# Optimization experiments

Measured on AMD Instinct MI355X. Metric: run time of the kernel, lower is better.

The kernel has to match this reference:

```python
import jax, jax.numpy as jnp
import numpy as np

BIG = jnp.float32(9e15)


def _normalize(sim, mask):
    # min/max are taken over positions where mask == 0 (faithful to the torch code)
    mn = jnp.min(jnp.where(mask == 0.0, sim, BIG), axis=-1, keepdims=True)
    mx = jnp.max(jnp.where(mask == 0.0, sim, -BIG), axis=-1, keepdims=True)
    return (sim - mn) / (mx - mn)


def setup_inputs() -> dict:
    key = jax.random.key(0)
    k1, k2 = jax.random.split(key)
    B, M = 4096, 8192
    return {
        "similarity_matrix": jax.random.normal(k1, (B, B), dtype=jnp.float32),
        "memory_bank_matrix": jax.random.normal(k2, (B, M), dtype=jnp.float32),
        "num_neighbors": 32,
        "temperature": jnp.ones((), dtype=jnp.float32),
    }


def reference(similarity_matrix, memory_bank_matrix, num_neighbors, temperature):
    sim = similarity_matrix
    B = sim.shape[0]
    eye = jnp.eye(B, dtype=sim.dtype)

    # --- neighbor masks via top-k over off-diagonal similarities ---
    sim_noself = jnp.where(eye == 0.0, sim, -BIG)
    _, topk_idx = jax.lax.top_k(sim_noself, num_neighbors)       # [B, k]
    rows = jnp.broadcast_to(jnp.arange(B)[:, None], topk_idx.shape)
    neighbor_mask = jnp.zeros((B, B), dtype=sim.dtype).at[rows, topk_idx].set(1.0)
    extended_mask = eye.at[rows, topk_idx].set(1.0)

    # --- centrality from memory bank ---
    centrality = jnp.mean(memory_bank_matrix, axis=-1)           # [B]
    cent_exp = jnp.broadcast_to(centrality[None, :], (B, B))

    norm_sim = _normalize(sim, extended_mask)
    norm_cent = _normalize(cent_exp, extended_mask)

    adjusted = jnp.where(neighbor_mask == 1.0, norm_sim - norm_cent, -BIG)

    # --- positive weights ---
    pw = jax.nn.softmax(adjusted * temperature, axis=-1)
    pw = jnp.where(neighbor_mask == 1.0, pw, 0.0)
    pw = jnp.where(eye == 1.0, 1.0, pw)  # fill_diagonal_(1.0)

    # --- masked log-softmax loss ---
    masked_sim = jnp.where(extended_mask == 1.0, sim, -BIG)
    logp = jax.nn.log_softmax(masked_sim, axis=-1) * pw
    per_row = -jnp.sum(logp, axis=-1) / jnp.sum(pw, axis=-1)
    return jnp.mean(per_row)
```

## Files before the change

kernel.cpp:

```cpp
#include <hip/hip_runtime.h>
#include <cmath>


#define CAP 256
#define MAXIT 40

__device__ inline float wave_max_f(float x) {
#pragma unroll
    for (int off = 32; off > 0; off >>= 1) x = fmaxf(x, __shfl_xor(x, off, 64));
    return x;
}
__device__ inline float wave_min_f(float x) {
#pragma unroll
    for (int off = 32; off > 0; off >>= 1) x = fminf(x, __shfl_xor(x, off, 64));
    return x;
}
__device__ inline float wave_sum_f(float x) {
#pragma unroll
    for (int off = 32; off > 0; off >>= 1) x += __shfl_xor(x, off, 64);
    return x;
}
__device__ inline unsigned int wave_min_u32(unsigned int x) {
#pragma unroll
    for (int off = 32; off > 0; off >>= 1) {
        unsigned int o = (unsigned int)__shfl_xor((int)x, off, 64);
        x = (o < x) ? o : x;
    }
    return x;
}

__device__ inline unsigned int f_to_key(float f) {
    unsigned int u = __float_as_uint(f);
    return u ^ ((u & 0x80000000u) ? 0xFFFFFFFFu : 0x80000000u);
}
__device__ inline float key_to_f(unsigned int key) {
    unsigned int u = key ^ ((key & 0x80000000u) ? 0x80000000u : 0xFFFFFFFFu);
    return __uint_as_float(u);
}

__device__ inline unsigned int lane_prefix(unsigned long long mask) {
    return __builtin_amdgcn_mbcnt_hi((unsigned int)(mask >> 32),
           __builtin_amdgcn_mbcnt_lo((unsigned int)mask, 0u));
}

__global__ __launch_bounds__(256)
void cent_kernel(const float* __restrict__ mem, float* __restrict__ cent, int M) {
    __shared__ float s[4];
    const int row = blockIdx.x;
    const float4* p = (const float4*)(mem + (size_t)row * M);
    const int n4 = M >> 2;
    float acc = 0.0f;
    int i = threadIdx.x;
    for (; i + 1792 < n4; i += 2048) {
        float4 q0 = p[i], q1 = p[i + 256], q2 = p[i + 512], q3 = p[i + 768];
        float4 q4 = p[i + 1024], q5 = p[i + 1280], q6 = p[i + 1536], q7 = p[i + 1792];
        acc += ((q0.x + q0.y) + (q0.z + q0.w)) + ((q1.x + q1.y) + (q1.z + q1.w))
             + ((q2.x + q2.y) + (q2.z + q2.w)) + ((q3.x + q3.y) + (q3.z + q3.w))
             + ((q4.x + q4.y) + (q4.z + q4.w)) + ((q5.x + q5.y) + (q5.z + q5.w))
             + ((q6.x + q6.y) + (q6.z + q6.w)) + ((q7.x + q7.y) + (q7.z + q7.w));
    }
    for (; i < n4; i += 256) {
        float4 q = p[i];
        acc += (q.x + q.y) + (q.z + q.w);
    }
    acc = wave_sum_f(acc);
    const int lane = threadIdx.x & 63, wid = threadIdx.x >> 6;
    if (lane == 0) s[wid] = acc;
    __syncthreads();
    if (threadIdx.x == 0) cent[row] = (s[0] + s[1] + s[2] + s[3]) / (float)M;
}

__global__ __launch_bounds__(256)
void row_loss_kernel(const float* __restrict__ sim,
                     const float* __restrict__ cent,
                     const int* __restrict__ knn,
                     const float* __restrict__ temp_p,
                     float* __restrict__ per_row, int B) {
    __shared__ __align__(16) unsigned long long cand[CAP];
    __shared__ unsigned long long s_sel[64];
    __shared__ unsigned long long s_p33;
    __shared__ unsigned int s_kmin[4];
    __shared__ float s_cmin[4], s_cmax[4];
    __shared__ float s_cmin2[4], s_cmax2[4];
    __shared__ unsigned int s_wcnt[4];
    __shared__ float s_diag;

    const int row = blockIdx.x, tid = threadIdx.x;
    const int lane = tid & 63, wid = tid >> 6;
    const int   k    = knn[0];
    const float temp = temp_p[0];

    const float4* rp = (const float4*)(sim + (size_t)row * B);
    const float4* cp = (const float4*)cent;
    float4 q0 = rp[tid], q1 = rp[256 + tid], q2 = rp[512 + tid], q3 = rp[768 + tid];
    float4 v0 = cp[tid], v1 = cp[256 + tid], v2 = cp[512 + tid], v3 = cp[768 + tid];

    unsigned int keys[16];
    float cv[16];
    unsigned int kmin = 0xFFFFFFFFu;
    {
        float t[16] = {q0.x, q0.y, q0.z, q0.w, q1.x, q1.y, q1.z, q1.w,
                       q2.x, q2.y, q2.z, q2.w, q3.x, q3.y, q3.z, q3.w};
        float c[16] = {v0.x, v0.y, v0.z, v0.w, v1.x, v1.y, v1.z, v1.w,
                       v2.x, v2.y, v2.z, v2.w, v3.x, v3.y, v3.z, v3.w};
#pragma unroll
        for (int c4i = 0; c4i < 4; ++c4i) {
#pragma unroll
            for (int m = 0; m < 4; ++m) {
                const int e = c4i * 4 + m;
                const int j = c4i * 1024 + tid * 4 + m;
                unsigned int key = f_to_key(t[e]);
                if (j == row) { s_diag = t[e]; key = 0u; }
                else if (key < kmin) kmin = key;
                keys[e] = key;
                cv[e] = c[e];
            }
        }
    }
    { unsigned int w = wave_min_u32(kmin); if (lane == 0) s_kmin[wid] = w; }

    unsigned int keyT = f_to_key(2.0f), loK = 0u, hiK = 0xFFFFFFFFu, cnt = 0;
    const unsigned int need = (unsigned int)k + 1u;
    for (int it = 0; it < MAXIT; ++it) {
        float cmin = INFINITY, cmax = -INFINITY;
        unsigned int wvCnt = 0;
#pragma unroll
        for (int e = 0; e < 16; ++e) {
            const unsigned int key = keys[e];
            const bool p = (key > keyT);
            const unsigned long long mask = __ballot(p);
            wvCnt += (unsigned int)__popcll(mask);
            if (!p && key != 0u) {
                cmin = fminf(cmin, cv[e]);
                cmax = fmaxf(cmax, cv[e]);
            }
        }
        { float a = wave_min_f(cmin), b = wave_max_f(cmax);
          if (lane == 0) { s_cmin[wid] = a; s_cmax[wid] = b; s_wcnt[wid] = wvCnt; } }
        __syncthreads();
        cnt = s_wcnt[0] + s_wcnt[1] + s_wcnt[2] + s_wcnt[3];
        if (cnt >= need && cnt <= CAP) break;
        if (it == MAXIT - 1) break;
        if (cnt < need) { hiK = keyT; keyT = loK + ((keyT - loK) >> 1); }
        else            { loK = keyT; keyT = keyT + ((hiK - keyT) >> 1); }
        __syncthreads();
    }

    {
        unsigned int base = 0;
#pragma unroll
        for (int w = 0; w < 4; ++w) if (w < wid) base += s_wcnt[w];
        unsigned int run = 0;
#pragma unroll
        for (int e = 0; e < 16; ++e) {
            const unsigned int key = keys[e];
            const bool p = (key > keyT);
            const unsigned long long mask = __ballot(p);
            if (p) {
                const unsigned int pos = base + run + lane_prefix(mask);
                if (pos < CAP)
                    cand[pos] = ((unsigned long long)key << 32) |
                                (unsigned long long)(0xFFFFFFFFu -
                                    (unsigned int)((e >> 2) * 1024 + tid * 4 + (e & 3)));
            }
            run += (unsigned int)__popcll(mask);
        }
        if (tid == 0) s_p33 = ((unsigned long long)1u) << 32;
        __syncthreads();
    }

    {
        const unsigned int n = min(cnt, (unsigned int)CAP);
        const unsigned int uk = (unsigned int)k;
        float cmin2 = INFINITY, cmax2 = -INFINITY;
        if ((unsigned int)(wid << 6) < n) {
            unsigned long long own = 0ull;
            if ((unsigned int)tid < n) own = cand[tid];
            unsigned int r = 0;
            const ulonglong2* c2 = (const ulonglong2*)cand;
            const unsigned int nq = n >> 2;
            for (unsigned int o = 0; o < nq; ++o) {
                ulonglong2 a0 = c2[2 * o], a1 = c2[2 * o + 1];
                r += (a0.x > own) ? 1u : 0u; r += (a0.y > own) ? 1u : 0u;
                r += (a1.x > own) ? 1u : 0u; r += (a1.y > own) ? 1u : 0u;
            }
            for (unsigned int i = nq << 2; i < n; ++i)
                r += (cand[i] > own) ? 1u : 0u;

            if ((unsigned int)tid < n) {
                if (r < uk) s_sel[r] = own;
                else if (r == uk) s_p33 = own;
                if (r >= uk) {
                    const int jj = (int)(0xFFFFFFFFu - (unsigned int)own);
                    const float cvv = cent[jj];
                    cmin2 = fminf(cmin2, cvv);
                    cmax2 = fmaxf(cmax2, cvv);
                }
            }
        }
        cmin2 = wave_min_f(cmin2);
        cmax2 = wave_max_f(cmax2);
        if (lane == 0) { s_cmin2[wid] = cmin2; s_cmax2[wid] = cmax2; }
        __syncthreads();
    }
    if (wid != 0) return;

    {
        const float sdiag = s_diag;
        const bool  act = (lane < k);
        const unsigned long long sel = act ? s_sel[lane] : 0ull;
        const float sj = act ? key_to_f((unsigned int)(sel >> 32)) : -INFINITY;
        const int   j  = act ? (int)(0xFFFFFFFFu - (unsigned int)sel) : 0;
        const float cj = cent[j];

        const float mn_c = fminf(
            fminf(fminf(s_cmin2[0], s_cmin2[1]), fminf(s_cmin2[2], s_cmin2[3])),
            fminf(fminf(s_cmin[0], s_cmin[1]), fminf(s_cmin[2], s_cmin[3])));
        const float mx_c = fmaxf(
            fmaxf(fmaxf(s_cmax2[0], s_cmax2[1]), fmaxf(s_cmax2[2], s_cmax2[3])),
            fmaxf(fmaxf(s_cmax[0], s_cmax[1]), fmaxf(s_cmax[2], s_cmax[3])));
        const unsigned int kminb =
            min(min(s_kmin[0], s_kmin[1]), min(s_kmin[2], s_kmin[3]));
        const float mn_s = key_to_f(kminb);
        const float mx_s = key_to_f((unsigned int)(s_p33 >> 32));

        float a = -INFINITY;
        if (act) {
            const float ns = (sj - mn_s) / (mx_s - mn_s);
            const float nc = (cj - mn_c) / (mx_c - mn_c);
            a = (ns - nc) * temp;
        }
        const float am   = wave_max_f(a);
        const float e    = act ? expf(a - am) : 0.0f;
        const float esum = wave_sum_f(e);
        const float pw   = e / esum;

        const float m2  = fmaxf(wave_max_f(sj), sdiag);
        const float ex  = act ? expf(sj - m2) : 0.0f;
        const float lse = m2 + logf(wave_sum_f(ex) + expf(sdiag - m2));

        const float num = wave_sum_f(act ? pw * (sj - lse) : 0.0f) + (sdiag - lse);
        const float den = 1.0f + wave_sum_f(pw);
        if (lane == 0) per_row[row] = -num / den;
    }
}

__global__ __launch_bounds__(256)
void reduce_kernel(const float* __restrict__ per_row, float* __restrict__ out, int B) {
    __shared__ float s[4];
    float acc = 0.0f;
    const float4* p = (const float4*)per_row;
    const int n4 = B >> 2;
    for (int i = threadIdx.x; i < n4; i += 256) {
        float4 q = p[i];
        acc += (q.x + q.y) + (q.z + q.w);
    }
    acc = wave_sum_f(acc);
    const int lane = threadIdx.x & 63, wid = threadIdx.x >> 6;
    if (lane == 0) s[wid] = acc;
    __syncthreads();
    if (threadIdx.x == 0) out[0] = (s[0] + s[1] + s[2] + s[3]) / (float)B;
}

extern "C" void kernel_launch(void* const* d_in, const int* in_sizes, int n_in,
                              void* d_out, int out_size, void* d_ws, size_t ws_size,
                              hipStream_t stream) {
    const float* sim  = (const float*)d_in[0];
    const float* mem  = (const float*)d_in[1];
    const int*   knn  = (const int*)d_in[2];
    const float* temp = (const float*)d_in[3];
    float* out     = (float*)d_out;
    float* cent    = (float*)d_ws;
    float* per_row = (float*)d_ws + 4096;

    const int B = (int)(std::sqrt((double)in_sizes[0]) + 0.5);
    const int M = in_sizes[1] / B;

    cent_kernel<<<B, 256, 0, stream>>>(mem, cent, M);
    row_loss_kernel<<<B, 256, 0, stream>>>(sim, cent, knn, temp, per_row, B);
    reduce_kernel<<<1, 256, 0, stream>>>(per_row, out, B);
}
```

Baseline: 51.73 us.

## Fuse first threshold pass with per-wave candidate compaction to skip extra sync

The first threshold count pass now writes candidates directly into per-wave 64-entry segments of the candidate buffer, with the initial threshold raised to 2.2. When the count lands in range and every wave fits its segment, the separate compaction pass and its barrier are skipped, and ranking walks the segments. The binary search runs only as a fallback. The row max for the log-sum-exp is also taken from the top selected key instead of a wave reduction. The cost is more branching and a data-dependent fast path tuned to the normal-distributed test data.

Result: faster. 50.63 us (-2.1%).

```diff
diff --git a/kernel.cpp b/kernel.cpp
--- a/kernel.cpp
+++ b/kernel.cpp
@@ -118,10 +118,11 @@
         }
     }
     { unsigned int w = wave_min_u32(kmin); if (lane == 0) s_kmin[wid] = w; }
-
-    unsigned int keyT = f_to_key(2.0f), loK = 0u, hiK = 0xFFFFFFFFu, cnt = 0;
+    if (tid == 0) s_p33 = ((unsigned long long)1u) << 32;
+
+    unsigned int keyT = f_to_key(2.2f), cnt = 0;
     const unsigned int need = (unsigned int)k + 1u;
-    for (int it = 0; it < MAXIT; ++it) {
+    {
         float cmin = INFINITY, cmax = -INFINITY;
         unsigned int wvCnt = 0;
 #pragma unroll
@@ -129,24 +130,55 @@
             const unsigned int key = keys[e];
             const bool p = (key > keyT);
             const unsigned long long mask = __ballot(p);
-            wvCnt += (unsigned int)__popcll(mask);
-            if (!p && key != 0u) {
+            if (p) {
+                const unsigned int pos = wvCnt + lane_prefix(mask);
+                if (pos < 64u)
+                    cand[(wid << 6) + pos] = ((unsigned long long)key << 32) |
+                        (unsigned long long)(0xFFFFFFFFu -
+                            (unsigned int)((e >> 2) * 1024 + tid * 4 + (e & 3)));
+            } else if (key != 0u) {
                 cmin = fminf(cmin, cv[e]);
                 cmax = fmaxf(cmax, cv[e]);
             }
-        }
-        { float a = wave_min_f(cmin), b = wave_max_f(cmax);
-          if (lane == 0) { s_cmin[wid] = a; s_cmax[wid] = b; s_wcnt[wid] = wvCnt; } }
-        __syncthreads();
-        cnt = s_wcnt[0] + s_wcnt[1] + s_wcnt[2] + s_wcnt[3];
-        if (cnt >= need && cnt <= CAP) break;
-        if (it == MAXIT - 1) break;
-        if (cnt < need) { hiK = keyT; keyT = loK + ((keyT - loK) >> 1); }
-        else            { loK = keyT; keyT = keyT + ((hiK - keyT) >> 1); }
-        __syncthreads();
-    }
-
-    {
+            wvCnt += (unsigned int)__popcll(mask);
+        }
+        float a = wave_min_f(cmin), b = wave_max_f(cmax);
+        if (lane == 0) { s_cmin[wid] = a; s_cmax[wid] = b; s_wcnt[wid] = wvCnt; }
+    }
+    __syncthreads();
+
+    unsigned int c0 = s_wcnt[0], c1 = s_wcnt[1], c2 = s_wcnt[2], c3 = s_wcnt[3];
+    cnt = c0 + c1 + c2 + c3;
+    bool cntOK = (cnt >= need && cnt <= CAP);
+    bool seg = cntOK && (c0 <= 64u) && (c1 <= 64u) && (c2 <= 64u) && (c3 <= 64u);
+
+    if (!seg) {
+        if (!cntOK) {
+            unsigned int loK = 0u, hiK = 0xFFFFFFFFu;
+            for (int it = 0; it < MAXIT; ++it) {
+                if (cnt < need) { hiK = keyT; keyT = loK + ((keyT - loK) >> 1); }
+                else            { loK = keyT; keyT = keyT + ((hiK - keyT) >> 1); }
+                __syncthreads();
+                float cmin = INFINITY, cmax = -INFINITY;
+                unsigned int wvCnt = 0;
+#pragma unroll
+                for (int e = 0; e < 16; ++e) {
+                    const unsigned int key = keys[e];
+                    const bool p = (key > keyT);
+                    wvCnt += (unsigned int)__popcll(__ballot(p));
+                    if (!p && key != 0u) {
+                        cmin = fminf(cmin, cv[e]);
+                        cmax = fmaxf(cmax, cv[e]);
+                    }
+                }
+                float a = wave_min_f(cmin), b = wave_max_f(cmax);
+                if (lane == 0) { s_cmin[wid] = a; s_cmax[wid] = b; s_wcnt[wid] = wvCnt; }
+                __syncthreads();
+                cnt = s_wcnt[0] + s_wcnt[1] + s_wcnt[2] + s_wcnt[3];
+                if (cnt >= need && cnt <= CAP) break;
+            }
+            c0 = s_wcnt[0]; c1 = s_wcnt[1]; c2 = s_wcnt[2]; c3 = s_wcnt[3];
+        }
         unsigned int base = 0;
 #pragma unroll
         for (int w = 0; w < 4; ++w) if (w < wid) base += s_wcnt[w];
@@ -160,34 +192,48 @@
                 const unsigned int pos = base + run + lane_prefix(mask);
                 if (pos < CAP)
                     cand[pos] = ((unsigned long long)key << 32) |
-                                (unsigned long long)(0xFFFFFFFFu -
-                                    (unsigned int)((e >> 2) * 1024 + tid * 4 + (e & 3)));
+                        (unsigned long long)(0xFFFFFFFFu -
+                            (unsigned int)((e >> 2) * 1024 + tid * 4 + (e & 3)));
             }
             run += (unsigned int)__popcll(mask);
         }
-        if (tid == 0) s_p33 = ((unsigned long long)1u) << 32;
         __syncthreads();
     }
 
     {
         const unsigned int n = min(cnt, (unsigned int)CAP);
         const unsigned int uk = (unsigned int)k;
+        const unsigned int e1 = c0, e2 = c0 + c1, e3 = c0 + c1 + c2;
         float cmin2 = INFINITY, cmax2 = -INFINITY;
         if ((unsigned int)(wid << 6) < n) {
             unsigned long long own = 0ull;
-            if ((unsigned int)tid < n) own = cand[tid];
+            const unsigned int t = (unsigned int)tid;
+            if (t < n) {
+                if (seg) {
+                    unsigned int w, off;
+                    if (t < e1)      { w = 0u; off = t; }
+                    else if (t < e2) { w = 1u; off = t - e1; }
+                    else if (t < e3) { w = 2u; off = t - e2; }
+                    else             { w = 3u; off = t - e3; }
+                    own = cand[(w << 6) + off];
+                } else {
+                    own = cand[t];
+                }
+            }
             unsigned int r = 0;
-            const ulonglong2* c2 = (const ulonglong2*)cand;
-            const unsigned int nq = n >> 2;
-            for (unsigned int o = 0; o < nq; ++o) {
-                ulonglong2 a0 = c2[2 * o], a1 = c2[2 * o + 1];
-                r += (a0.x > own) ? 1u : 0u; r += (a0.y > own) ? 1u : 0u;
-                r += (a1.x > own) ? 1u : 0u; r += (a1.y > own) ? 1u : 0u;
-            }
-            for (unsigned int i = nq << 2; i < n; ++i)
-                r += (cand[i] > own) ? 1u : 0u;
-
-            if ((unsigned int)tid < n) {
+            if (seg) {
+#pragma unroll
+                for (int w = 0; w < 4; ++w) {
+                    const unsigned int len = s_wcnt[w];
+                    const unsigned int b = (unsigned int)(w << 6);
+                    for (unsigned int i = 0; i < len; ++i)
+                        r += (cand[b + i] > own) ? 1u : 0u;
+                }
+            } else {
+                for (unsigned int i = 0; i < n; ++i)
+                    r += (cand[i] > own) ? 1u : 0u;
+            }
+            if (t < n) {
                 if (r < uk) s_sel[r] = own;
                 else if (r == uk) s_p33 = own;
                 if (r >= uk) {
@@ -235,7 +281,7 @@
         const float esum = wave_sum_f(e);
         const float pw   = e / esum;
 
-        const float m2  = fmaxf(wave_max_f(sj), sdiag);
+        const float m2  = fmaxf(key_to_f((unsigned int)(s_sel[0] >> 32)), sdiag);
         const float ex  = act ? expf(sj - m2) : 0.0f;
         const float lse = m2 + logf(wave_sum_f(ex) + expf(sdiag - m2));
 
```
